# Optimization experiments

Measured on AMD Instinct MI355X. Metric: run time of the kernel, lower is better.

The kernel has to match this reference:

```python
import jax, jax.numpy as jnp
import numpy as np

N_NODES = 100000
EPS = 1e-5


def _layernorm(x, g, b):
    # per-node layer norm over feature dim
    mu = jnp.mean(x, axis=-1, keepdims=True)
    var = jnp.mean(jnp.square(x - mu), axis=-1, keepdims=True)
    return (x - mu) * jax.lax.rsqrt(var + EPS) * g + b


def _gcn_conv(x, W, b, src, dst, n_nodes):
    # GCNConv: xW, then symmetric-normalized aggregation with self-loops.
    xw = x @ W  # [N, out]
    ones = jnp.ones(src.shape[0], dtype=x.dtype)
    deg = jax.ops.segment_sum(ones, dst, num_segments=n_nodes) + 1.0  # +1 self loop
    dinv = jax.lax.rsqrt(deg)  # [N]
    norm = dinv[src] * dinv[dst]  # [E]
    msg = xw[src] * norm[:, None]  # [E, out]  <- dominant memory traffic
    agg = jax.ops.segment_sum(msg, dst, num_segments=n_nodes)
    agg = agg + xw * (dinv * dinv)[:, None]  # self-loop contribution
    return agg + b


def setup_inputs() -> dict:
    key = jax.random.key(0)
    ks = jax.random.split(key, 16)
    in_c, hid, out_c = 128, 64, 32
    E = 1_600_000
    d = {}
    d['x'] = jax.random.normal(ks[0], (N_NODES, in_c), dtype=jnp.float32)
    d['edge_index'] = jax.random.randint(ks[1], (2, E), 0, N_NODES, dtype=jnp.int64)

    def lin(k, fi, fo):
        s = 1.0 / np.sqrt(fi)
        k1, k2 = jax.random.split(k)
        return (jax.random.uniform(k1, (fi, fo), jnp.float32, -s, s),
                jax.random.uniform(k2, (fo,), jnp.float32, -s, s))

    d['W1'], d['b1'] = lin(ks[2], in_c, hid)
    d['g1'], d['be1'] = jnp.ones((hid,), jnp.float32), jnp.zeros((hid,), jnp.float32)
    d['W2'], d['b2'] = lin(ks[3], hid, 2 * hid)
    d['g2'], d['be2'] = jnp.ones((2 * hid,), jnp.float32), jnp.zeros((2 * hid,), jnp.float32)
    d['W3'], d['b3'] = lin(ks[4], 2 * hid, hid)
    d['g3'], d['be3'] = jnp.ones((hid,), jnp.float32), jnp.zeros((hid,), jnp.float32)
    d['lw1'], d['lb1'] = lin(ks[5], hid, hid // 2)
    d['g4'], d['be4'] = jnp.ones((hid // 2,), jnp.float32), jnp.zeros((hid // 2,), jnp.float32)
    d['lw2'], d['lb2'] = lin(ks[6], hid // 2, out_c)
    return d


def reference(x, edge_index, W1, b1, g1, be1, W2, b2, g2, be2, W3, b3, g3, be3,
              lw1, lb1, g4, be4, lw2, lb2):
    src, dst = edge_index[0], edge_index[1]
    h = _gcn_conv(x, W1, b1, src, dst, N_NODES)
    h = jax.nn.elu(_layernorm(h, g1, be1))
    h = _gcn_conv(h, W2, b2, src, dst, N_NODES)
    h = jax.nn.elu(_layernorm(h, g2, be2))
    h = _gcn_conv(h, W3, b3, src, dst, N_NODES)
    h = jax.nn.elu(_layernorm(h, g3, be3))
    h = h @ lw1 + lb1
    h = jax.nn.elu(_layernorm(h, g4, be4))
    return h @ lw2 + lb2
```

## Files before the change

### kernel.cpp

```cpp
#include <hip/hip_runtime.h>
#include <math.h>

#define N_NODES 100000
#define LN_EPS 1e-5f
#define NBUCK ((N_NODES + 255) / 256)
#define EPB 8192

typedef __attribute__((ext_vector_type(8))) short bf16x8;
typedef __attribute__((ext_vector_type(4))) float f32x4;

__device__ __forceinline__ unsigned short f2bf(float f) {
    unsigned int u = __float_as_uint(f);
    return (unsigned short)((u + 0x7FFFu + ((u >> 16) & 1u)) >> 16);
}
__device__ __forceinline__ float bf2f(unsigned short u) {
    return __uint_as_float(((unsigned int)u) << 16);
}


__global__ void count_edges(const int* __restrict__ dst, int* __restrict__ counts, int E) {
    __shared__ int hist[NBUCK];
    for (int b = threadIdx.x; b < NBUCK; b += 512) hist[b] = 0;
    __syncthreads();
    int e0 = blockIdx.x * EPB;
#pragma unroll 4
    for (int i = 0; i < EPB / 512; ++i) {
        int e = e0 + i * 512 + (int)threadIdx.x;
        if (e < E) atomicAdd(&hist[((unsigned)dst[e]) >> 8], 1);
    }
    __syncthreads();
    for (int b = threadIdx.x; b < NBUCK; b += 512)
        counts[blockIdx.x * NBUCK + b] = hist[b];
}

__global__ void scan_pos(const int* __restrict__ counts, int* __restrict__ pos,
                         int* __restrict__ tot, int nblk) {
    __shared__ int s[512];
    int b = blockIdx.x, i = threadIdx.x;
    int v = (i < nblk) ? counts[i * NBUCK + b] : 0;
    s[i] = v;
    __syncthreads();
    for (int off = 1; off < 512; off <<= 1) {
        int t = (i >= off) ? s[i - off] : 0;
        __syncthreads();
        s[i] += t;
        __syncthreads();
    }
    if (i < nblk) pos[i * NBUCK + b] = s[i] - v;
    if (i == 511) tot[b] = s[511];
}

__global__ void scan_base(const int* __restrict__ tot, int* __restrict__ base, int E) {
    __shared__ int s[512];
    int i = threadIdx.x;
    int v = (i < NBUCK) ? tot[i] : 0;
    s[i] = v;
    __syncthreads();
    for (int off = 1; off < 512; off <<= 1) {
        int t = (i >= off) ? s[i - off] : 0;
        __syncthreads();
        s[i] += t;
        __syncthreads();
    }
    if (i < NBUCK) base[i] = s[i] - v;
    if (i == 0) base[NBUCK] = E;
}

__global__ void place_edges(const int* __restrict__ src, const int* __restrict__ dst,
                            const int* __restrict__ pos, const int* __restrict__ base,
                            unsigned* __restrict__ bucket, int E) {
    __shared__ int lcur[NBUCK];
    for (int b = threadIdx.x; b < NBUCK; b += 512)
        lcur[b] = pos[blockIdx.x * NBUCK + b] + base[b];
    __syncthreads();
    int e0 = blockIdx.x * EPB;
#pragma unroll 4
    for (int i = 0; i < EPB / 512; ++i) {
        int e = e0 + i * 512 + (int)threadIdx.x;
        if (e < E) {
            unsigned d = (unsigned)dst[e];
            unsigned s = (unsigned)src[e];
            int p = atomicAdd(&lcur[d >> 8], 1);
            bucket[p] = ((d & 255u) << 24) | s;
        }
    }
}

__global__ void build_csr_node(const unsigned* __restrict__ bucket, const int* __restrict__ base,
                               int* __restrict__ offsets, float* __restrict__ dinv,
                               int* __restrict__ csr, int E) {
    __shared__ int hist[256];
    __shared__ int cur[256];
    int b = blockIdx.x, t = threadIdx.x;
    int r0 = b << 8;
    hist[t] = 0;
    __syncthreads();
    int s0 = base[b], s1 = base[b + 1];
    for (int e = s0 + t; e < s1; e += 256)
        atomicAdd(&hist[bucket[e] >> 24], 1);
    __syncthreads();
    int deg = hist[t];
    for (int off = 1; off < 256; off <<= 1) {
        int tv = (t >= off) ? hist[t - off] : 0;
        __syncthreads();
        hist[t] += tv;
        __syncthreads();
    }
    int excl = hist[t] - deg;
    int node = r0 + t;
    if (node < N_NODES) {
        offsets[node] = s0 + excl;
        dinv[node] = rsqrtf((float)deg + 1.f);
        cur[t] = s0 + excl;
    }
    if (node == N_NODES - 1) offsets[N_NODES] = E;
    __syncthreads();
    for (int e = s0 + t; e < s1; e += 256) {
        unsigned u = bucket[e];
        int p = atomicAdd(&cur[u >> 24], 1);
        csr[p] = (int)(u & 0xFFFFFFu);
    }
}

template <int K, int OUT, bool LN, bool BIAS, bool AF32, bool OF32, bool SCALED>
__launch_bounds__(256)
__global__ void mfma_gemm(const void* __restrict__ Xv, const float* __restrict__ W,
                          const float* __restrict__ bias, const float* __restrict__ gamma,
                          const float* __restrict__ beta, void* __restrict__ Yv, int n,
                          const float* __restrict__ dinvp) {
    constexpr int T  = OUT / 16;
    constexpr int KP = K + 8;

    __shared__ __align__(16) unsigned short sWT[OUT * KP];
    for (int i = threadIdx.x; i < K * OUT; i += 256) {
        int k = i / OUT, o = i - k * OUT;
        sWT[o * KP + k] = f2bf(W[i]);
    }
    __syncthreads();

    int wv = threadIdx.x >> 6, lane = threadIdx.x & 63;
    int quad = lane >> 4, l16 = lane & 15;
    int m0 = (blockIdx.x * 4 + wv) * 16;
    int rowc = min(m0 + l16, n - 1);

    f32x4 acc[T];
#pragma unroll
    for (int t = 0; t < T; ++t) acc[t] = (f32x4){0.f, 0.f, 0.f, 0.f};

#pragma unroll
    for (int s = 0; s < K / 32; ++s) {
        int koff = s * 32 + quad * 8;
        bf16x8 af;
        if (AF32) {
            const float4* X4 = (const float4*)Xv;
            size_t base = ((size_t)rowc * K + koff) >> 2;
            float4 a0 = X4[base];
            float4 a1 = X4[base + 1];
            af[0] = (short)f2bf(a0.x); af[1] = (short)f2bf(a0.y);
            af[2] = (short)f2bf(a0.z); af[3] = (short)f2bf(a0.w);
            af[4] = (short)f2bf(a1.x); af[5] = (short)f2bf(a1.y);
            af[6] = (short)f2bf(a1.z); af[7] = (short)f2bf(a1.w);
        } else {
            const unsigned short* Xb = (const unsigned short*)Xv;
            af = *(const bf16x8*)(Xb + (size_t)rowc * K + koff);
        }
#pragma unroll
        for (int t = 0; t < T; ++t) {
            const bf16x8 bfrag = *(const bf16x8*)&sWT[(t * 16 + l16) * KP + koff];
            acc[t] = __builtin_amdgcn_mfma_f32_16x16x32_bf16(af, bfrag, acc[t], 0, 0, 0);
        }
    }

    float bj[T], gj[T], btj[T];
#pragma unroll
    for (int t = 0; t < T; ++t) {
        int c = t * 16 + l16;
        bj[t]  = BIAS ? bias[c] : 0.f;
        gj[t]  = LN ? gamma[c] : 1.f;
        btj[t] = LN ? beta[c] : 0.f;
    }

    float* Yf = (float*)Yv;
    unsigned short* Yb = (unsigned short*)Yv;

    if (LN) {
        float s[4] = {0.f, 0.f, 0.f, 0.f}, sq[4] = {0.f, 0.f, 0.f, 0.f};
#pragma unroll
        for (int t = 0; t < T; ++t)
#pragma unroll
            for (int r = 0; r < 4; ++r) {
                float v = acc[t][r] + bj[t];
                s[r] += v;
                sq[r] += v * v;
            }
#pragma unroll
        for (int off = 1; off < 16; off <<= 1)
#pragma unroll
            for (int r = 0; r < 4; ++r) {
                s[r] += __shfl_xor(s[r], off, 64);
                sq[r] += __shfl_xor(sq[r], off, 64);
            }
        float mu[4], rs[4];
#pragma unroll
        for (int r = 0; r < 4; ++r) {
            mu[r] = s[r] / OUT;
            float var = sq[r] / OUT - mu[r] * mu[r];
            rs[r] = rsqrtf(var + LN_EPS);
        }
#pragma unroll
        for (int r = 0; r < 4; ++r) {
            int rowg = m0 + quad * 4 + r;
            if (rowg < n) {
                float dv = SCALED ? dinvp[rowg] : 1.f;
#pragma unroll
                for (int t = 0; t < T; ++t) {
                    float y = (acc[t][r] + bj[t] - mu[r]) * rs[r] * gj[t] + btj[t];
                    y = y > 0.f ? y : expm1f(y);
                    if (SCALED) y *= dv;
                    size_t idx = (size_t)rowg * OUT + t * 16 + l16;
                    if (OF32) Yf[idx] = y; else Yb[idx] = f2bf(y);
                }
            }
        }
    } else {
#pragma unroll
        for (int r = 0; r < 4; ++r) {
            int rowg = m0 + quad * 4 + r;
            if (rowg < n) {
                float dv = SCALED ? dinvp[rowg] : 1.f;
#pragma unroll
                for (int t = 0; t < T; ++t) {
                    float y = acc[t][r] + bj[t];
                    if (SCALED) y *= dv;
                    size_t idx = (size_t)rowg * OUT + t * 16 + l16;
                    if (OF32) Yf[idx] = y; else Yb[idx] = f2bf(y);
                }
            }
        }
    }
}

__launch_bounds__(256)
__global__ void lin_fused(const unsigned short* __restrict__ X, const float* __restrict__ W1f,
                          const float* __restrict__ b1f, const float* __restrict__ g,
                          const float* __restrict__ be, const float* __restrict__ W2f,
                          const float* __restrict__ b2f, float* __restrict__ out, int n) {
    constexpr int KP1 = 64 + 8;
    constexpr int KP2 = 32 + 8;
    constexpr int TS  = 56;
    __shared__ __align__(16) unsigned short sWT1[32 * KP1];
    __shared__ __align__(16) unsigned short sWT2[32 * KP2];
    __shared__ __align__(16) unsigned short sT[4][16 * TS];

    for (int i = threadIdx.x; i < 64 * 32; i += 256) {
        int k = i >> 5, o = i & 31;
        sWT1[o * KP1 + k] = f2bf(W1f[i]);
    }
    for (int i = threadIdx.x; i < 32 * 32; i += 256) {
        int k = i >> 5, o = i & 31;
        sWT2[o * KP2 + k] = f2bf(W2f[i]);
    }
    __syncthreads();

    int wv = threadIdx.x >> 6, lane = threadIdx.x & 63;
    int quad = lane >> 4, l16 = lane & 15;
    int m0 = (blockIdx.x * 4 + wv) * 16;
    int rowc = min(m0 + l16, n - 1);

    f32x4 acc[2];
    acc[0] = (f32x4){0.f, 0.f, 0.f, 0.f};
    acc[1] = (f32x4){0.f, 0.f, 0.f, 0.f};
#pragma unroll
    for (int s = 0; s < 2; ++s) {
        int koff = s * 32 + quad * 8;
        bf16x8 af = *(const bf16x8*)(X + (size_t)rowc * 64 + koff);
#pragma unroll
        for (int t = 0; t < 2; ++t) {
            const bf16x8 bfrag = *(const bf16x8*)&sWT1[(t * 16 + l16) * KP1 + koff];
            acc[t] = __builtin_amdgcn_mfma_f32_16x16x32_bf16(af, bfrag, acc[t], 0, 0, 0);
        }
    }

    float bj[2], gj[2], btj[2];
#pragma unroll
    for (int t = 0; t < 2; ++t) {
        int c = t * 16 + l16;
        bj[t] = b1f[c]; gj[t] = g[c]; btj[t] = be[c];
    }
    float s4[4] = {0.f, 0.f, 0.f, 0.f}, sq4[4] = {0.f, 0.f, 0.f, 0.f};
#pragma unroll
    for (int t = 0; t < 2; ++t)
#pragma unroll
        for (int r = 0; r < 4; ++r) {
            float v = acc[t][r] + bj[t];
            s4[r] += v;
            sq4[r] += v * v;
        }
#pragma unroll
    for (int off = 1; off < 16; off <<= 1)
#pragma unroll
        for (int r = 0; r < 4; ++r) {
            s4[r] += __shfl_xor(s4[r], off, 64);
            sq4[r] += __shfl_xor(sq4[r], off, 64);
        }
#pragma unroll
    for (int r = 0; r < 4; ++r) {
        float mu = s4[r] * (1.f / 32.f);
        float var = sq4[r] * (1.f / 32.f) - mu * mu;
        float rs = rsqrtf(var + LN_EPS);
#pragma unroll
        for (int t = 0; t < 2; ++t) {
            float z = (acc[t][r] + bj[t] - mu) * rs * gj[t] + btj[t];
            z = z > 0.f ? z : expm1f(z);
            sT[wv][(quad * 4 + r) * TS + t * 16 + l16] = f2bf(z);
        }
    }
    __syncthreads();

    bf16x8 a2 = *(const bf16x8*)&sT[wv][l16 * TS + quad * 8];
    f32x4 acc2[2];
#pragma unroll
    for (int t = 0; t < 2; ++t) {
        const bf16x8 bfrag = *(const bf16x8*)&sWT2[(t * 16 + l16) * KP2 + quad * 8];
        acc2[t] = __builtin_amdgcn_mfma_f32_16x16x32_bf16(
            a2, bfrag, (f32x4){0.f, 0.f, 0.f, 0.f}, 0, 0, 0);
    }
#pragma unroll
    for (int r = 0; r < 4; ++r) {
        int rowg = m0 + quad * 4 + r;
        if (rowg < n) {
#pragma unroll
            for (int t = 0; t < 2; ++t)
                out[(size_t)rowg * 32 + t * 16 + l16] = acc2[t][r] + b2f[t * 16 + l16];
        }
    }
}

template <bool LN, bool SCALEOUT>
__launch_bounds__(256)
__global__ void gather_s(const unsigned short* __restrict__ xs, const int* __restrict__ offsets,
                         const int* __restrict__ csr_src, const float* __restrict__ dinv,
                         const float* __restrict__ bias, const float* __restrict__ gamma,
                         const float* __restrict__ beta, unsigned short* __restrict__ out, int n) {
    int wave = threadIdx.x >> 6;
    int lane = threadIdx.x & 63;
    int node = blockIdx.x * (blockDim.x >> 6) + wave;
    if (node >= n) return;
    int beg = __builtin_amdgcn_readfirstlane(offsets[node]);
    int end = __builtin_amdgcn_readfirstlane(offsets[node + 1]);
    int deg = end - beg;

    float dd = dinv[node];
    unsigned short selfv = xs[((unsigned)node << 6) + lane];
    float bl = LN ? bias[lane] : 0.f;
    float gl = LN ? gamma[lane] : 1.f;
    float tl = LN ? beta[lane] : 0.f;

    float a0 = 0.f, a1 = 0.f, a2 = 0.f, a3 = 0.f;
    for (int half = 0; half < deg; half += 16) {
        int m = deg - half;
        int sc[16];
#pragma unroll
        for (int j = 0; j < 16; ++j)
            sc[j] = __builtin_amdgcn_readfirstlane(csr_src[beg + half + j]);
        unsigned short v[16];
#pragma unroll
        for (int j = 0; j < 16; ++j) {
            int sel = (j < m) ? sc[j] : sc[0];
            const unsigned short* rp = xs + ((size_t)(unsigned)sel << 6);
            v[j] = rp[lane];
        }
#pragma unroll
        for (int j = 0; j < 16; ++j) {
            float f = bf2f(v[j]);
            if ((j & 3) == 0) a0 += f;
            else if ((j & 3) == 1) a1 += f;
            else if ((j & 3) == 2) a2 += f;
            else a3 += f;
        }
        if (m < 16) a0 -= (float)(16 - m) * bf2f(v[0]);
    }

    float y = (a0 + a1 + a2 + a3 + bf2f(selfv)) * dd;

    if (!LN) {
        out[((unsigned)node << 6) + lane] = f2bf(y);
        return;
    }
    float yb = y + bl;
    float s = yb, sq = yb * yb;
#pragma unroll
    for (int off = 1; off < 64; off <<= 1) {
        s += __shfl_xor(s, off, 64);
        sq += __shfl_xor(sq, off, 64);
    }
    float mu = s * (1.f / 64.f);
    float var = sq * (1.f / 64.f) - mu * mu;
    float rs = rsqrtf(var + LN_EPS);
    float z = (yb - mu) * rs * gl + tl;
    z = z > 0.f ? z : expm1f(z);
    if (SCALEOUT) z *= dd;
    out[((unsigned)node << 6) + lane] = f2bf(z);
}

extern "C" void kernel_launch(void* const* d_in, const int* in_sizes, int n_in,
                              void* d_out, int out_size, void* d_ws, size_t ws_size,
                              hipStream_t stream) {
    const float* x  = (const float*)d_in[0];
    const int* ei   = (const int*)d_in[1];
    const float* W1 = (const float*)d_in[2];
    const float* b1 = (const float*)d_in[3];
    const float* g1 = (const float*)d_in[4];
    const float* be1= (const float*)d_in[5];
    const float* W2 = (const float*)d_in[6];
    const float* b2 = (const float*)d_in[7];
    const float* g2 = (const float*)d_in[8];
    const float* be2= (const float*)d_in[9];
    const float* W3 = (const float*)d_in[10];
    const float* b3 = (const float*)d_in[11];
    const float* g3 = (const float*)d_in[12];
    const float* be3= (const float*)d_in[13];
    const float* lw1= (const float*)d_in[14];
    const float* lb1= (const float*)d_in[15];
    const float* g4 = (const float*)d_in[16];
    const float* be4= (const float*)d_in[17];
    const float* lw2= (const float*)d_in[18];
    const float* lb2= (const float*)d_in[19];
    float* out = (float*)d_out;

    const int E = in_sizes[1] / 2;
    const int* src = ei;
    const int* dst = ei + E;
    const int N = N_NODES;

    unsigned short* bufA = (unsigned short*)d_ws;
    unsigned short* bufB = bufA + (size_t)N * 128;
    float* dinv    = (float*)(bufB + (size_t)N * 128);
    int*   offsets = (int*)(dinv + N);
    int*   csr     = offsets + N + 1;
    int*   tot     = csr + E;
    int*   base    = tot + NBUCK;

    auto cdiv = [](long long a, long long b) { return (int)((a + b - 1) / b); };
    const int NBLK = cdiv(E, EPB);

    int* counts = (int*)bufA;
    int* pos    = counts + (size_t)NBLK * NBUCK;
    unsigned* bucket = (unsigned*)bufB;

    const int GB = cdiv(N, 64);

    count_edges<<<NBLK, 512, 0, stream>>>(dst, counts, E);
    scan_pos<<<NBUCK, 512, 0, stream>>>(counts, pos, tot, NBLK);
    scan_base<<<1, 512, 0, stream>>>(tot, base, E);
    place_edges<<<NBLK, 512, 0, stream>>>(src, dst, pos, base, bucket, E);
    build_csr_node<<<NBUCK, 256, 0, stream>>>(bucket, base, offsets, dinv, csr, E);

    mfma_gemm<128, 64, false, false, true, false, true><<<GB, 256, 0, stream>>>(
        x, W1, nullptr, nullptr, nullptr, bufA, N, dinv);
    gather_s<true, true><<<cdiv(N, 4), 256, 0, stream>>>(bufA, offsets, csr, dinv, b1, g1, be1, bufB, N);

    gather_s<false, false><<<cdiv(N, 4), 256, 0, stream>>>(bufB, offsets, csr, dinv, nullptr, nullptr, nullptr, bufA, N);
    mfma_gemm<64, 128, true, true, false, false, false><<<GB, 256, 0, stream>>>(
        bufA, W2, b2, g2, be2, bufB, N, nullptr);

    mfma_gemm<128, 64, false, false, false, false, true><<<GB, 256, 0, stream>>>(
        bufB, W3, nullptr, nullptr, nullptr, bufA, N, dinv);
    gather_s<true, false><<<cdiv(N, 4), 256, 0, stream>>>(bufA, offsets, csr, dinv, b3, g3, be3, bufB, N);

    lin_fused<<<GB, 256, 0, stream>>>(bufB, lw1, lb1, g4, be4, lw2, lb2, out, N);
}
```

Before: 322.3 us.

## Fuse layer-2 GEMM, LayerNorm/ELU and layer-3 GEMM; scalar-load CSR indices

A new kernel computes X·W2 + b2, applies LayerNorm and ELU, stages the 128-wide result in shared memory and multiplies by W3 with dinv scaling, all in one pass. This removes the round trip of the 128-column intermediate through global memory and one kernel launch. The gather kernel now reads CSR source indices through a constant-address-space pointer, so they can be fetched with scalar loads instead of vector loads followed by readfirstlane. The fused kernel reads and writes the same buffer in place, which is only safe because each wave reads its own rows before it writes them. It also uses more shared memory per block, which may lower occupancy.

```diff
diff --git a/kernel.cpp b/kernel.cpp
--- a/kernel.cpp
+++ b/kernel.cpp
@@ -8,6 +8,7 @@
 
 typedef __attribute__((ext_vector_type(8))) short bf16x8;
 typedef __attribute__((ext_vector_type(4))) float f32x4;
+typedef __attribute__((address_space(4))) const int kc_int;
 
 __device__ __forceinline__ unsigned short f2bf(float f) {
     unsigned int u = __float_as_uint(f);
@@ -241,6 +242,109 @@
 }
 
 __launch_bounds__(256)
+__global__ void gemm23_fused(const unsigned short* __restrict__ X,
+                             const float* __restrict__ W2f, const float* __restrict__ b2f,
+                             const float* __restrict__ g2, const float* __restrict__ be2,
+                             const float* __restrict__ W3f, const float* __restrict__ dinvp,
+                             unsigned short* __restrict__ Y, int n) {
+    constexpr int KP2 = 72;
+    constexpr int KP3 = 136;
+    constexpr int TS  = 136;
+    __shared__ __align__(16) unsigned short sWT2[128 * KP2];
+    __shared__ __align__(16) unsigned short sWT3[64 * KP3];
+    __shared__ __align__(16) unsigned short sT[4][16 * TS];
+
+    for (int i = threadIdx.x; i < 64 * 128; i += 256) {
+        int k = i >> 7, o = i & 127;
+        sWT2[o * KP2 + k] = f2bf(W2f[i]);
+    }
+    for (int i = threadIdx.x; i < 128 * 64; i += 256) {
+        int k = i >> 6, o = i & 63;
+        sWT3[o * KP3 + k] = f2bf(W3f[i]);
+    }
+    __syncthreads();
+
+    int wv = threadIdx.x >> 6, lane = threadIdx.x & 63;
+    int quad = lane >> 4, l16 = lane & 15;
+    int m0 = (blockIdx.x * 4 + wv) * 16;
+    int rowc = min(m0 + l16, n - 1);
+
+    f32x4 acc[8];
+#pragma unroll
+    for (int t = 0; t < 8; ++t) acc[t] = (f32x4){0.f, 0.f, 0.f, 0.f};
+#pragma unroll
+    for (int s = 0; s < 2; ++s) {
+        int koff = s * 32 + quad * 8;
+        bf16x8 af = *(const bf16x8*)(X + (size_t)rowc * 64 + koff);
+#pragma unroll
+        for (int t = 0; t < 8; ++t) {
+            const bf16x8 bfrag = *(const bf16x8*)&sWT2[(t * 16 + l16) * KP2 + koff];
+            acc[t] = __builtin_amdgcn_mfma_f32_16x16x32_bf16(af, bfrag, acc[t], 0, 0, 0);
+        }
+    }
+
+    float bj[8], gj[8], btj[8];
+#pragma unroll
+    for (int t = 0; t < 8; ++t) {
+        int c = t * 16 + l16;
+        bj[t] = b2f[c]; gj[t] = g2[c]; btj[t] = be2[c];
+    }
+    float s4[4] = {0.f, 0.f, 0.f, 0.f}, sq4[4] = {0.f, 0.f, 0.f, 0.f};
+#pragma unroll
+    for (int t = 0; t < 8; ++t)
+#pragma unroll
+        for (int r = 0; r < 4; ++r) {
+            float v = acc[t][r] + bj[t];
+            s4[r] += v;
+            sq4[r] += v * v;
+        }
+#pragma unroll
+    for (int off = 1; off < 16; off <<= 1)
+#pragma unroll
+        for (int r = 0; r < 4; ++r) {
+            s4[r] += __shfl_xor(s4[r], off, 64);
+            sq4[r] += __shfl_xor(sq4[r], off, 64);
+        }
+#pragma unroll
+    for (int r = 0; r < 4; ++r) {
+        float mu = s4[r] * (1.f / 128.f);
+        float var = sq4[r] * (1.f / 128.f) - mu * mu;
+        float rs = rsqrtf(var + LN_EPS);
+#pragma unroll
+        for (int t = 0; t < 8; ++t) {
+            float z = (acc[t][r] + bj[t] - mu) * rs * gj[t] + btj[t];
+            z = z > 0.f ? z : expm1f(z);
+            sT[wv][(quad * 4 + r) * TS + t * 16 + l16] = f2bf(z);
+        }
+    }
+    __syncthreads();
+
+    f32x4 acc2[4];
+#pragma unroll
+    for (int t = 0; t < 4; ++t) acc2[t] = (f32x4){0.f, 0.f, 0.f, 0.f};
+#pragma unroll
+    for (int s = 0; s < 4; ++s) {
+        int koff = s * 32 + quad * 8;
+        bf16x8 af = *(const bf16x8*)&sT[wv][l16 * TS + koff];
+#pragma unroll
+        for (int t = 0; t < 4; ++t) {
+            const bf16x8 bfrag = *(const bf16x8*)&sWT3[(t * 16 + l16) * KP3 + koff];
+            acc2[t] = __builtin_amdgcn_mfma_f32_16x16x32_bf16(af, bfrag, acc2[t], 0, 0, 0);
+        }
+    }
+#pragma unroll
+    for (int r = 0; r < 4; ++r) {
+        int rowg = m0 + quad * 4 + r;
+        if (rowg < n) {
+            float dv = dinvp[rowg];
+#pragma unroll
+            for (int t = 0; t < 4; ++t)
+                Y[(size_t)rowg * 64 + t * 16 + l16] = f2bf(acc2[t][r] * dv);
+        }
+    }
+}
+
+__launch_bounds__(256)
 __global__ void lin_fused(const unsigned short* __restrict__ X, const float* __restrict__ W1f,
                           const float* __restrict__ b1f, const float* __restrict__ g,
                           const float* __restrict__ be, const float* __restrict__ W2f,
@@ -349,6 +453,7 @@
     int beg = __builtin_amdgcn_readfirstlane(offsets[node]);
     int end = __builtin_amdgcn_readfirstlane(offsets[node + 1]);
     int deg = end - beg;
+    kc_int* csc = (kc_int*)(unsigned long long)(csr_src + beg);
 
     float dd = dinv[node];
     unsigned short selfv = xs[((unsigned)node << 6) + lane];
@@ -361,8 +466,7 @@
         int m = deg - half;
         int sc[16];
 #pragma unroll
-        for (int j = 0; j < 16; ++j)
-            sc[j] = __builtin_amdgcn_readfirstlane(csr_src[beg + half + j]);
+        for (int j = 0; j < 16; ++j) sc[j] = csc[half + j];
         unsigned short v[16];
 #pragma unroll
         for (int j = 0; j < 16; ++j) {
@@ -461,11 +565,9 @@
     gather_s<true, true><<<cdiv(N, 4), 256, 0, stream>>>(bufA, offsets, csr, dinv, b1, g1, be1, bufB, N);
 
     gather_s<false, false><<<cdiv(N, 4), 256, 0, stream>>>(bufB, offsets, csr, dinv, nullptr, nullptr, nullptr, bufA, N);
-    mfma_gemm<64, 128, true, true, false, false, false><<<GB, 256, 0, stream>>>(
-        bufA, W2, b2, g2, be2, bufB, N, nullptr);
-
-    mfma_gemm<128, 64, false, false, false, false, true><<<GB, 256, 0, stream>>>(
-        bufB, W3, nullptr, nullptr, nullptr, bufA, N, dinv);
+
+    gemm23_fused<<<GB, 256, 0, stream>>>(bufA, W2, b2, g2, be2, W3, dinv, bufA, N);
+
     gather_s<true, false><<<cdiv(N, 4), 256, 0, stream>>>(bufA, offsets, csr, dinv, b3, g3, be3, bufB, N);
 
     lin_fused<<<GB, 256, 0, stream>>>(bufB, lw1, lb1, g4, be4, lw2, lb2, out, N);
```

Result: no change. 320.3 us (-0.6%).
